# Optimization experiments

Measured on AMD Instinct MI355X. Metric: run time of the kernel, lower is better.

Reference implementation:

```python
import jax, jax.numpy as jnp
import numpy as np

LOG_STD_MAX = 2.0
LOG_STD_MIN = -5.0
N_EXPERTS = 16
TOPK = 4
OBS = 512
ACT = 256
BATCH = 16384


def setup_inputs() -> dict:
    key = jax.random.key(0)
    ks = jax.random.split(key, 7)
    s_obs = 1.0 / np.sqrt(OBS)
    return {
        "x": jax.random.normal(ks[0], (BATCH, OBS), dtype=jnp.float32),
        "router_w": jax.random.uniform(ks[1], (N_EXPERTS, OBS), jnp.float32, -s_obs, s_obs),
        "router_b": jax.random.uniform(ks[2], (N_EXPERTS,), jnp.float32, -s_obs, s_obs),
        "mean_w": jax.random.uniform(ks[3], (N_EXPERTS, ACT, OBS), jnp.float32, -s_obs, s_obs),
        "mean_b": jax.random.uniform(ks[4], (N_EXPERTS, ACT), jnp.float32, -s_obs, s_obs),
        "log_std_w": jax.random.uniform(ks[5], (N_EXPERTS, ACT, OBS), jnp.float32, -s_obs, s_obs),
        "log_std_b": jax.random.uniform(ks[6], (N_EXPERTS, ACT), jnp.float32, -s_obs, s_obs),
        "router_noise": 0,
    }


def reference(x, router_w, router_b, mean_w, mean_b, log_std_w, log_std_b, router_noise):
    # router_noise=0 -> deterministic path (training-time noise omitted)
    B = x.shape[0]
    router_logits = x @ router_w.T + router_b                    # [B, E]
    router_probs = jax.nn.softmax(router_logits, axis=-1)         # [B, E]
    topk_probs, topk_idx = jax.lax.top_k(router_probs, TOPK)      # [B, K]
    sparse_probs = jnp.zeros_like(router_probs).at[
        jnp.arange(B)[:, None], topk_idx
    ].set(topk_probs)                                             # [B, E]

    # all-expert dense stack: [B, E, A]
    expert_out = jnp.einsum("bo,eao->bea", x, mean_w) + mean_b
    log_std_out = jnp.einsum("bo,eao->bea", x, log_std_w) + log_std_b

    w = sparse_probs[:, :, None]                                  # [B, E, 1]
    mean = jnp.sum(expert_out * w, axis=1)                        # [B, A]
    log_std = jnp.sum(log_std_out * w, axis=1)                    # [B, A]
    log_std = jnp.tanh(log_std)
    log_std = LOG_STD_MIN + 0.5 * (LOG_STD_MAX - LOG_STD_MIN) * (log_std + 1.0)
    return mean, log_std
```

## Files before the change

kernel.cpp:

```cpp
#include <hip/hip_runtime.h>
#include <math.h>

#define BB   16384
#define OBS  512
#define NE   16
#define ACTD 256
#define TK   4

#define WS_ROWLIST_OFF  ((size_t)64)
#define WS_PROBLIST_OFF (WS_ROWLIST_OFF + (size_t)NE * BB * 4)
#define WS_SLOT_OFF     (WS_PROBLIST_OFF + (size_t)NE * BB * 4)
#define WS_XBF_OFF      (WS_SLOT_OFF + (size_t)NE * BB * 4)
#define WS_WM_OFF       (WS_XBF_OFF + (size_t)BB * OBS * 2)
#define WS_WL_OFF       (WS_WM_OFF + (size_t)NE * ACTD * OBS * 2)
#define WS_PART_OFF     (WS_WL_OFF + (size_t)NE * ACTD * OBS * 2)
#define WS_NEEDED_A2    (WS_PART_OFF + (size_t)2 * BB * TK * ACTD * 2)

typedef __attribute__((ext_vector_type(8))) short short8;
typedef __attribute__((ext_vector_type(4))) float floatx4;

__device__ __forceinline__ ushort f2bf(float f) {
    union { float f; unsigned u; } v; v.f = f;
    unsigned r = v.u + 0x7fffu + ((v.u >> 16) & 1u);
    return (ushort)(r >> 16);
}
__device__ __forceinline__ float bf2f(ushort u) {
    union { unsigned u; float f; } v; v.u = ((unsigned)u) << 16;
    return v.f;
}
__device__ __forceinline__ float lstd_act(float v) {
    return -5.f + 7.f * __builtin_amdgcn_rcpf(1.f + __expf(-2.f * v));
}

__global__ __launch_bounds__(256) void cvt2_bf16(
    const float* __restrict__ s0, const float* __restrict__ s1,
    ushort* __restrict__ d0, ushort* __restrict__ d1, int n4,
    int* __restrict__ counts)
{
    if (blockIdx.x == 0 && threadIdx.x < NE) counts[threadIdx.x] = 0;
    const int i = blockIdx.x * 256 + threadIdx.x;
    const float4* src = (i < n4) ? ((const float4*)s0 + i) : ((const float4*)s1 + (i - n4));
    ushort4* dst = (i < n4) ? ((ushort4*)d0 + i) : ((ushort4*)d1 + (i - n4));
    float4 v = *src;
    ushort4 o;
    o.x = f2bf(v.x); o.y = f2bf(v.y); o.z = f2bf(v.z); o.w = f2bf(v.w);
    *dst = o;
}

__global__ __launch_bounds__(256) void router_kernel(
    const float* __restrict__ x, const float* __restrict__ rw,
    const float* __restrict__ rb,
    int* __restrict__ counts, int* __restrict__ rowlist,
    float* __restrict__ problist, int* __restrict__ slot_of,
    ushort* __restrict__ xbf, int do_aux)
{
    __shared__ float wlds[NE * OBS];
    __shared__ int   lcnt[NE], lbase[NE];
    __shared__ int   s_e[64], s_lpos[64];
    __shared__ float s_p[64];

    const float4* rw4 = (const float4*)rw;
    float4* wl4 = (float4*)wlds;
    #pragma unroll
    for (int i = 0; i < 8; ++i) wl4[threadIdx.x + 256 * i] = rw4[threadIdx.x + 256 * i];
    if (threadIdx.x < NE) lcnt[threadIdx.x] = 0;
    __syncthreads();

    const int wave = threadIdx.x >> 6;
    const int lane = threadIdx.x & 63;
    const int q    = lane >> 4;
    const int i16  = lane & 15;
    const int row  = blockIdx.x * 16 + wave * 4 + q;

    const float4* xr = (const float4*)(x + (size_t)row * OBS);
    float4 xv[8];
    #pragma unroll
    for (int s = 0; s < 8; ++s) xv[s] = xr[s * 16 + i16];

    if (do_aux) {
        ushort4* xo = (ushort4*)(xbf + (size_t)row * OBS);
        #pragma unroll
        for (int s = 0; s < 8; ++s) {
            ushort4 o;
            o.x = f2bf(xv[s].x); o.y = f2bf(xv[s].y);
            o.z = f2bf(xv[s].z); o.w = f2bf(xv[s].w);
            xo[s * 16 + i16] = o;
        }
    }

    float p[NE];
    float m = -1e30f;
    #pragma unroll
    for (int e = 0; e < NE; ++e) {
        const float4* wep = (const float4*)(wlds + e * OBS);
        float d = 0.f;
        #pragma unroll
        for (int s = 0; s < 8; ++s) {
            float4 wv = wep[s * 16 + i16];
            d += xv[s].x * wv.x + xv[s].y * wv.y + xv[s].z * wv.z + xv[s].w * wv.w;
        }
        d += __shfl_xor(d, 1, 64);
        d += __shfl_xor(d, 2, 64);
        d += __shfl_xor(d, 4, 64);
        d += __shfl_xor(d, 8, 64);
        d += rb[e];
        p[e] = d;
        m = fmaxf(m, d);
    }
    float s = 0.f;
    #pragma unroll
    for (int e = 0; e < NE; ++e) { p[e] = __expf(p[e] - m); s += p[e]; }
    const float inv = 1.f / s;
    #pragma unroll
    for (int e = 0; e < NE; ++e) p[e] *= inv;

    int   sel_e[TK];
    float sel_p[TK];
    #pragma unroll
    for (int k = 0; k < TK; ++k) {
        float best = -1.f; int be = 0;
        #pragma unroll
        for (int e = 0; e < NE; ++e)
            if (p[e] > best) { best = p[e]; be = e; }
        sel_e[k] = be; sel_p[k] = best;
        #pragma unroll
        for (int e = 0; e < NE; ++e)
            if (e == be) p[e] = -2.f;
    }
    if (i16 < TK) {
        const int e = sel_e[i16];
        const int lpos = atomicAdd(&lcnt[e], 1);
        const int sid = (wave * 4 + q) * 4 + i16;
        s_e[sid] = e; s_p[sid] = sel_p[i16]; s_lpos[sid] = lpos;
    }
    __syncthreads();
    if (threadIdx.x < NE)
        lbase[threadIdx.x] = atomicAdd(&counts[threadIdx.x], lcnt[threadIdx.x]);
    __syncthreads();
    if (threadIdx.x < 64) {
        const int sid = threadIdx.x;
        const int e   = s_e[sid];
        const int pos = lbase[e] + s_lpos[sid];
        const int grow = blockIdx.x * 16 + (sid >> 2);
        rowlist[e * BB + pos]  = grow;
        problist[e * BB + pos] = s_p[sid];
        if (do_aux) slot_of[e * BB + pos] = grow * TK + (sid & 3);
    }
}

__global__ __launch_bounds__(256) void moe_gemm_64(
    const ushort* __restrict__ xbf,
    const ushort* __restrict__ wmean, const ushort* __restrict__ wlstd,
    const float* __restrict__ mean_b, const float* __restrict__ lstd_b,
    const int* __restrict__ counts, const int* __restrict__ rowlist,
    const float* __restrict__ problist, const int* __restrict__ slot_of,
    ushort* __restrict__ partial)
{
    const int flat = blockIdx.x + 256 * blockIdx.y + 4096 * blockIdx.z;
    const int virt = (flat & 7) * 2048 + (flat >> 3);
    const int zz    = virt & 3;
    const int tile0 = ((virt >> 2) & 255) * 64;
    const int e     = virt >> 10;

    const int cnt = counts[e];
    if (tile0 >= cnt) return;

    const int which = zz >> 1;
    const int ctile = (zz & 1) * 128;
    const ushort* W   = (which ? wlstd : wmean) + (size_t)e * ACTD * OBS;
    const float* bias = (which ? lstd_b : mean_b) + e * ACTD + ctile;
    ushort* Pp = partial + (size_t)which * BB * TK * ACTD;

    __shared__ __align__(16) ushort xls[64 * 64];
    __shared__ __align__(16) ushort wls[128 * 64];
    __shared__ int   idx_l[64];
    __shared__ float probs_l[64];

    const int tid = threadIdx.x;
    const int l   = tid & 63;
    const int w   = tid >> 6;

    if (tid < 64) {
        const int pos = tile0 + tid;
        const bool v = pos < cnt;
        probs_l[tid] = v ? problist[e * BB + pos] : 0.f;
        idx_l[tid]   = v ? slot_of[e * BB + pos] : -1;
    }

    const int c_sw = (l & 7) ^ (l >> 3);
    const ushort* xp[2];
    #pragma unroll
    for (int i = 0; i < 2; ++i) {
        const int lrow = 16 * w + 8 * i + (l >> 3);
        const int pos  = tile0 + lrow;
        const int grow = (pos < cnt) ? rowlist[e * BB + pos] : rowlist[e * BB + tile0];
        xp[i] = xbf + (size_t)grow * OBS + c_sw * 8;
    }
    const ushort* wp[4];
    #pragma unroll
    for (int j = 0; j < 4; ++j) {
        const int col = ctile + 32 * w + 8 * j + (l >> 3);
        wp[j] = W + (size_t)col * OBS + c_sw * 8;
    }

    const int wm  = (w >> 1) * 32;
    const int wn  = (w & 1) * 64;
    const int rlo = l & 15;
    const int q   = l >> 4;
    const int r7  = rlo & 7;

    floatx4 acc[2][4];
    #pragma unroll
    for (int mi = 0; mi < 2; ++mi)
        #pragma unroll
        for (int ni = 0; ni < 4; ++ni)
            acc[mi][ni] = (floatx4){0.f, 0.f, 0.f, 0.f};

    for (int kt = 0; kt < OBS; kt += 64) {
        __syncthreads();
        #pragma unroll
        for (int i = 0; i < 2; ++i)
            __builtin_amdgcn_global_load_lds(
                (const __attribute__((address_space(1))) unsigned int*)(xp[i] + kt),
                (__attribute__((address_space(3))) unsigned int*)(xls + (2 * w + i) * 512),
                16, 0, 0);
        #pragma unroll
        for (int j = 0; j < 4; ++j)
            __builtin_amdgcn_global_load_lds(
                (const __attribute__((address_space(1))) unsigned int*)(wp[j] + kt),
                (__attribute__((address_space(3))) unsigned int*)(wls + (4 * w + j) * 512),
                16, 0, 0);
        __syncthreads();

        #pragma unroll
        for (int ks = 0; ks < 2; ++ks) {
            const int ch = (4 * ks + q) ^ r7;
            short8 af[2], bfr[4];
            #pragma unroll
            for (int mi = 0; mi < 2; ++mi)
                af[mi] = *(const short8*)(xls + (wm + mi * 16 + rlo) * 64 + ch * 8);
            #pragma unroll
            for (int ni = 0; ni < 4; ++ni)
                bfr[ni] = *(const short8*)(wls + (wn + ni * 16 + rlo) * 64 + ch * 8);
            #pragma unroll
            for (int mi = 0; mi < 2; ++mi)
                #pragma unroll
                for (int ni = 0; ni < 4; ++ni)
                    acc[mi][ni] = __builtin_amdgcn_mfma_f32_16x16x32_bf16(
                        af[mi], bfr[ni], acc[mi][ni], 0, 0, 0);
        }
    }

    #pragma unroll
    for (int mi = 0; mi < 2; ++mi) {
        #pragma unroll
        for (int r = 0; r < 4; ++r) {
            const int lrow = wm + mi * 16 + q * 4 + r;
            const int slot = idx_l[lrow];
            if (slot < 0) continue;
            const float pw = probs_l[lrow];
            ushort* orow = Pp + (size_t)slot * ACTD + ctile + wn + rlo;
            #pragma unroll
            for (int ni = 0; ni < 4; ++ni)
                orow[ni * 16] = f2bf(pw * (acc[mi][ni][r] + bias[wn + ni * 16 + rlo]));
        }
    }
}

__global__ __launch_bounds__(256) void combine_kernel(
    const ushort* __restrict__ partial, float* __restrict__ out)
{
    const int t  = blockIdx.x * 256 + threadIdx.x;
    const int r  = t >> 6;
    const int c4 = (t & 63) * 4;
    const ushort* Pm = partial;
    const ushort* Pl = partial + (size_t)BB * TK * ACTD;

    float m0 = 0.f, m1 = 0.f, m2 = 0.f, m3 = 0.f;
    float l0 = 0.f, l1 = 0.f, l2 = 0.f, l3 = 0.f;
    #pragma unroll
    for (int k = 0; k < TK; ++k) {
        const size_t off = (size_t)(r * TK + k) * ACTD + c4;
        ushort4 vm = *(const ushort4*)(Pm + off);
        ushort4 vl = *(const ushort4*)(Pl + off);
        m0 += bf2f(vm.x); m1 += bf2f(vm.y); m2 += bf2f(vm.z); m3 += bf2f(vm.w);
        l0 += bf2f(vl.x); l1 += bf2f(vl.y); l2 += bf2f(vl.z); l3 += bf2f(vl.w);
    }
    float4 mo = make_float4(m0, m1, m2, m3);
    float4 lo = make_float4(lstd_act(l0), lstd_act(l1), lstd_act(l2), lstd_act(l3));
    *(float4*)(out + (size_t)r * ACTD + c4) = mo;
    *(float4*)(out + (size_t)BB * ACTD + (size_t)r * ACTD + c4) = lo;
}

__global__ __launch_bounds__(256) void moe_gemm_f32(
    const float* __restrict__ x,
    const float* __restrict__ mean_w, const float* __restrict__ mean_b,
    const float* __restrict__ lstd_w, const float* __restrict__ lstd_b,
    const int* __restrict__ counts, const int* __restrict__ rowlist,
    const float* __restrict__ problist, float* __restrict__ out)
{
    const int e = blockIdx.y;
    const int cnt = counts[e];
    const int tile0 = blockIdx.x * 32;
    if (tile0 >= cnt) return;

    const int zz    = blockIdx.z;
    const int which = zz >> 1;
    const int ctile = (zz & 1) * 128;
    const float* W    = (which ? lstd_w : mean_w) + (size_t)e * ACTD * OBS;
    const float* bias = (which ? lstd_b : mean_b) + e * ACTD;
    float* outp = out + (size_t)which * BB * ACTD;

    __shared__ float xls[32][32];
    __shared__ float wls[32][128];

    const int sr  = threadIdx.x >> 3;
    const int skq = threadIdx.x & 7;
    int stage_row = -1;
    {
        const int pos = tile0 + sr;
        if (pos < cnt) stage_row = rowlist[e * BB + pos];
    }

    const int r0 = (threadIdx.x >> 5) << 2;
    const int c0 = (threadIdx.x & 31) << 2;

    float acc[4][4] = {};

    for (int kt = 0; kt < OBS; kt += 32) {
        __syncthreads();
        {
            float4 v = make_float4(0.f, 0.f, 0.f, 0.f);
            if (stage_row >= 0)
                v = *(const float4*)(x + (size_t)stage_row * OBS + kt + skq * 4);
            xls[skq * 4 + 0][sr] = v.x;
            xls[skq * 4 + 1][sr] = v.y;
            xls[skq * 4 + 2][sr] = v.z;
            xls[skq * 4 + 3][sr] = v.w;
        }
        #pragma unroll
        for (int j = 0; j < 4; ++j) {
            const int i  = threadIdx.x + 256 * j;
            const int c  = i >> 3;
            const int kq = i & 7;
            float4 v = *(const float4*)(W + (size_t)(ctile + c) * OBS + kt + kq * 4);
            wls[kq * 4 + 0][c] = v.x;
            wls[kq * 4 + 1][c] = v.y;
            wls[kq * 4 + 2][c] = v.z;
            wls[kq * 4 + 3][c] = v.w;
        }
        __syncthreads();

        #pragma unroll
        for (int k = 0; k < 32; ++k) {
            const float4 xa = *(const float4*)&xls[k][r0];
            const float4 wb = *(const float4*)&wls[k][c0];
            const float xv[4] = { xa.x, xa.y, xa.z, xa.w };
            const float wv[4] = { wb.x, wb.y, wb.z, wb.w };
            #pragma unroll
            for (int i = 0; i < 4; ++i)
                #pragma unroll
                for (int j = 0; j < 4; ++j)
                    acc[i][j] = fmaf(xv[i], wv[j], acc[i][j]);
        }
    }

    #pragma unroll
    for (int i = 0; i < 4; ++i) {
        const int pos = tile0 + r0 + i;
        if (pos >= cnt) break;
        const int grow = rowlist[e * BB + pos];
        const float pw = problist[e * BB + pos];
        float* orow = outp + (size_t)grow * ACTD + ctile + c0;
        #pragma unroll
        for (int j = 0; j < 4; ++j)
            atomicAdd(&orow[j], pw * (acc[i][j] + bias[ctile + c0 + j]));
    }
}

__global__ __launch_bounds__(256) void tanh_ep(float* __restrict__ out)
{
    const int i = blockIdx.x * 256 + threadIdx.x;
    float4* p = (float4*)(out + (size_t)BB * ACTD);
    float4 v = p[i];
    v.x = -5.f + 3.5f * (tanhf(v.x) + 1.f);
    v.y = -5.f + 3.5f * (tanhf(v.y) + 1.f);
    v.z = -5.f + 3.5f * (tanhf(v.z) + 1.f);
    v.w = -5.f + 3.5f * (tanhf(v.w) + 1.f);
    p[i] = v;
}

extern "C" void kernel_launch(void* const* d_in, const int* in_sizes, int n_in,
                              void* d_out, int out_size, void* d_ws, size_t ws_size,
                              hipStream_t stream)
{
    const float* x        = (const float*)d_in[0];
    const float* router_w = (const float*)d_in[1];
    const float* router_b = (const float*)d_in[2];
    const float* mean_w   = (const float*)d_in[3];
    const float* mean_b   = (const float*)d_in[4];
    const float* lstd_w   = (const float*)d_in[5];
    const float* lstd_b   = (const float*)d_in[6];

    float* out = (float*)d_out;
    int*    counts   = (int*)d_ws;
    int*    rowlist  = (int*)((char*)d_ws + WS_ROWLIST_OFF);
    float*  problist = (float*)((char*)d_ws + WS_PROBLIST_OFF);
    int*    slot_of  = (int*)((char*)d_ws + WS_SLOT_OFF);
    ushort* xbf      = (ushort*)((char*)d_ws + WS_XBF_OFF);
    ushort* wmbf     = (ushort*)((char*)d_ws + WS_WM_OFF);
    ushort* wlbf     = (ushort*)((char*)d_ws + WS_WL_OFF);
    ushort* partial  = (ushort*)((char*)d_ws + WS_PART_OFF);

    const bool tierA2 = (ws_size >= WS_NEEDED_A2);

    if (tierA2) {
        const int wn4 = NE * ACTD * OBS / 4;
        cvt2_bf16<<<2 * wn4 / 256, 256, 0, stream>>>(mean_w, lstd_w, wmbf, wlbf,
                                                     wn4, counts);

        router_kernel<<<BB / 16, 256, 0, stream>>>(x, router_w, router_b,
                                                   counts, rowlist, problist,
                                                   slot_of, xbf, 1);

        dim3 grid(BB / 64, NE, 4);
        moe_gemm_64<<<grid, 256, 0, stream>>>(xbf, wmbf, wlbf, mean_b, lstd_b,
                                              counts, rowlist, problist,
                                              slot_of, partial);
        combine_kernel<<<BB * 64 / 256, 256, 0, stream>>>(partial, out);
    } else {
        hipMemsetAsync(d_ws, 0, 64, stream);
        hipMemsetAsync(d_out, 0, (size_t)out_size * sizeof(float), stream);
        router_kernel<<<BB / 16, 256, 0, stream>>>(x, router_w, router_b,
                                                   counts, rowlist, problist,
                                                   (int*)nullptr, (ushort*)nullptr, 0);
        dim3 grid(BB / 32, NE, 4);
        moe_gemm_f32<<<grid, 256, 0, stream>>>(x, mean_w, mean_b, lstd_w, lstd_b,
                                               counts, rowlist, problist, out);
        tanh_ep<<<(BB * ACTD / 4) / 256, 256, 0, stream>>>(out);
    }
}
```

Measured before the change: 207.3 us.

## Fuse weight bf16 conversion into router and compute mean/log_std in one GEMM block

Removes the separate weight-conversion kernel by folding the fp32-to-bf16 weight conversion into the router kernel and replacing the counts reset with a memset. The GEMM now computes both the mean and the log_std projections per block, sharing each loaded x tile across two weight tiles and two accumulator sets. This halves the number of GEMM blocks and the gathered x loads, at the cost of more registers and LDS per block, which may lower occupancy.

```diff
diff --git a/kernel.cpp b/kernel.cpp
--- a/kernel.cpp
+++ b/kernel.cpp
@@ -32,27 +32,14 @@
     return -5.f + 7.f * __builtin_amdgcn_rcpf(1.f + __expf(-2.f * v));
 }
 
-__global__ __launch_bounds__(256) void cvt2_bf16(
-    const float* __restrict__ s0, const float* __restrict__ s1,
-    ushort* __restrict__ d0, ushort* __restrict__ d1, int n4,
-    int* __restrict__ counts)
-{
-    if (blockIdx.x == 0 && threadIdx.x < NE) counts[threadIdx.x] = 0;
-    const int i = blockIdx.x * 256 + threadIdx.x;
-    const float4* src = (i < n4) ? ((const float4*)s0 + i) : ((const float4*)s1 + (i - n4));
-    ushort4* dst = (i < n4) ? ((ushort4*)d0 + i) : ((ushort4*)d1 + (i - n4));
-    float4 v = *src;
-    ushort4 o;
-    o.x = f2bf(v.x); o.y = f2bf(v.y); o.z = f2bf(v.z); o.w = f2bf(v.w);
-    *dst = o;
-}
-
 __global__ __launch_bounds__(256) void router_kernel(
     const float* __restrict__ x, const float* __restrict__ rw,
     const float* __restrict__ rb,
     int* __restrict__ counts, int* __restrict__ rowlist,
     float* __restrict__ problist, int* __restrict__ slot_of,
-    ushort* __restrict__ xbf, int do_aux)
+    ushort* __restrict__ xbf,
+    const float* __restrict__ mwf, const float* __restrict__ lwf,
+    ushort* __restrict__ wmbf, ushort* __restrict__ wlbf, int do_aux)
 {
     __shared__ float wlds[NE * OBS];
     __shared__ int   lcnt[NE], lbase[NE];
@@ -146,9 +133,29 @@
         problist[e * BB + pos] = s_p[sid];
         if (do_aux) slot_of[e * BB + pos] = grow * TK + (sid & 3);
     }
-}
-
-__global__ __launch_bounds__(256) void moe_gemm_64(
+
+    if (do_aux) {
+        const int gid = blockIdx.x * 256 + threadIdx.x;
+        const float4* m4 = (const float4*)mwf;
+        const float4* l4 = (const float4*)lwf;
+        ushort4* mo = (ushort4*)wmbf;
+        ushort4* lo = (ushort4*)wlbf;
+        #pragma unroll
+        for (int j = 0; j < 2; ++j) {
+            const int idx = gid + 262144 * j;
+            float4 a = m4[idx];
+            ushort4 oa;
+            oa.x = f2bf(a.x); oa.y = f2bf(a.y); oa.z = f2bf(a.z); oa.w = f2bf(a.w);
+            mo[idx] = oa;
+            float4 b = l4[idx];
+            ushort4 ob;
+            ob.x = f2bf(b.x); ob.y = f2bf(b.y); ob.z = f2bf(b.z); ob.w = f2bf(b.w);
+            lo[idx] = ob;
+        }
+    }
+}
+
+__global__ __launch_bounds__(256) void moe_gemm_2t(
     const ushort* __restrict__ xbf,
     const ushort* __restrict__ wmean, const ushort* __restrict__ wlstd,
     const float* __restrict__ mean_b, const float* __restrict__ lstd_b,
@@ -157,22 +164,25 @@
     ushort* __restrict__ partial)
 {
     const int flat = blockIdx.x + 256 * blockIdx.y + 4096 * blockIdx.z;
-    const int virt = (flat & 7) * 2048 + (flat >> 3);
-    const int zz    = virt & 3;
-    const int tile0 = ((virt >> 2) & 255) * 64;
-    const int e     = virt >> 10;
+    const int virt = (flat & 7) * 1024 + (flat >> 3);
+    const int zz    = virt & 1;
+    const int tile0 = ((virt >> 1) & 255) * 64;
+    const int e     = virt >> 9;
 
     const int cnt = counts[e];
     if (tile0 >= cnt) return;
 
-    const int which = zz >> 1;
-    const int ctile = (zz & 1) * 128;
-    const ushort* W   = (which ? wlstd : wmean) + (size_t)e * ACTD * OBS;
-    const float* bias = (which ? lstd_b : mean_b) + e * ACTD + ctile;
-    ushort* Pp = partial + (size_t)which * BB * TK * ACTD;
+    const int ctile = zz * 128;
+    const ushort* Wm = wmean + (size_t)e * ACTD * OBS;
+    const ushort* Wl = wlstd + (size_t)e * ACTD * OBS;
+    const float* bm  = mean_b + e * ACTD + ctile;
+    const float* bl  = lstd_b + e * ACTD + ctile;
+    ushort* PpM = partial;
+    ushort* PpL = partial + (size_t)BB * TK * ACTD;
 
     __shared__ __align__(16) ushort xls[64 * 64];
-    __shared__ __align__(16) ushort wls[128 * 64];
+    __shared__ __align__(16) ushort wmls[128 * 64];
+    __shared__ __align__(16) ushort wlls[128 * 64];
     __shared__ int   idx_l[64];
     __shared__ float probs_l[64];
 
@@ -196,25 +206,30 @@
         const int grow = (pos < cnt) ? rowlist[e * BB + pos] : rowlist[e * BB + tile0];
         xp[i] = xbf + (size_t)grow * OBS + c_sw * 8;
     }
-    const ushort* wp[4];
+    const ushort* wpm[4];
+    const ushort* wpl[4];
     #pragma unroll
     for (int j = 0; j < 4; ++j) {
         const int col = ctile + 32 * w + 8 * j + (l >> 3);
-        wp[j] = W + (size_t)col * OBS + c_sw * 8;
-    }
-
-    const int wm  = (w >> 1) * 32;
-    const int wn  = (w & 1) * 64;
-    const int rlo = l & 15;
-    const int q   = l >> 4;
-    const int r7  = rlo & 7;
-
-    floatx4 acc[2][4];
+        const size_t off = (size_t)col * OBS + c_sw * 8;
+        wpm[j] = Wm + off;
+        wpl[j] = Wl + off;
+    }
+
+    const int wm_  = (w >> 1) * 32;
+    const int wn   = (w & 1) * 64;
+    const int rlo  = l & 15;
+    const int q    = l >> 4;
+    const int r7   = rlo & 7;
+
+    floatx4 accM[2][4], accL[2][4];
     #pragma unroll
     for (int mi = 0; mi < 2; ++mi)
         #pragma unroll
-        for (int ni = 0; ni < 4; ++ni)
-            acc[mi][ni] = (floatx4){0.f, 0.f, 0.f, 0.f};
+        for (int ni = 0; ni < 4; ++ni) {
+            accM[mi][ni] = (floatx4){0.f, 0.f, 0.f, 0.f};
+            accL[mi][ni] = (floatx4){0.f, 0.f, 0.f, 0.f};
+        }
 
     for (int kt = 0; kt < OBS; kt += 64) {
         __syncthreads();
@@ -227,8 +242,14 @@
         #pragma unroll
         for (int j = 0; j < 4; ++j)
             __builtin_amdgcn_global_load_lds(
-                (const __attribute__((address_space(1))) unsigned int*)(wp[j] + kt),
-                (__attribute__((address_space(3))) unsigned int*)(wls + (4 * w + j) * 512),
+                (const __attribute__((address_space(1))) unsigned int*)(wpm[j] + kt),
+                (__attribute__((address_space(3))) unsigned int*)(wmls + (4 * w + j) * 512),
+                16, 0, 0);
+        #pragma unroll
+        for (int j = 0; j < 4; ++j)
+            __builtin_amdgcn_global_load_lds(
+                (const __attribute__((address_space(1))) unsigned int*)(wpl[j] + kt),
+                (__attribute__((address_space(3))) unsigned int*)(wlls + (4 * w + j) * 512),
                 16, 0, 0);
         __syncthreads();
 
@@ -238,16 +259,25 @@
             short8 af[2], bfr[4];
             #pragma unroll
             for (int mi = 0; mi < 2; ++mi)
-                af[mi] = *(const short8*)(xls + (wm + mi * 16 + rlo) * 64 + ch * 8);
+                af[mi] = *(const short8*)(xls + (wm_ + mi * 16 + rlo) * 64 + ch * 8);
             #pragma unroll
             for (int ni = 0; ni < 4; ++ni)
-                bfr[ni] = *(const short8*)(wls + (wn + ni * 16 + rlo) * 64 + ch * 8);
+                bfr[ni] = *(const short8*)(wmls + (wn + ni * 16 + rlo) * 64 + ch * 8);
             #pragma unroll
             for (int mi = 0; mi < 2; ++mi)
                 #pragma unroll
                 for (int ni = 0; ni < 4; ++ni)
-                    acc[mi][ni] = __builtin_amdgcn_mfma_f32_16x16x32_bf16(
-                        af[mi], bfr[ni], acc[mi][ni], 0, 0, 0);
+                    accM[mi][ni] = __builtin_amdgcn_mfma_f32_16x16x32_bf16(
+                        af[mi], bfr[ni], accM[mi][ni], 0, 0, 0);
+            #pragma unroll
+            for (int ni = 0; ni < 4; ++ni)
+                bfr[ni] = *(const short8*)(wlls + (wn + ni * 16 + rlo) * 64 + ch * 8);
+            #pragma unroll
+            for (int mi = 0; mi < 2; ++mi)
+                #pragma unroll
+                for (int ni = 0; ni < 4; ++ni)
+                    accL[mi][ni] = __builtin_amdgcn_mfma_f32_16x16x32_bf16(
+                        af[mi], bfr[ni], accL[mi][ni], 0, 0, 0);
         }
     }
 
@@ -255,14 +285,18 @@
     for (int mi = 0; mi < 2; ++mi) {
         #pragma unroll
         for (int r = 0; r < 4; ++r) {
-            const int lrow = wm + mi * 16 + q * 4 + r;
+            const int lrow = wm_ + mi * 16 + q * 4 + r;
             const int slot = idx_l[lrow];
             if (slot < 0) continue;
             const float pw = probs_l[lrow];
-            ushort* orow = Pp + (size_t)slot * ACTD + ctile + wn + rlo;
-            #pragma unroll
-            for (int ni = 0; ni < 4; ++ni)
-                orow[ni * 16] = f2bf(pw * (acc[mi][ni][r] + bias[wn + ni * 16 + rlo]));
+            const size_t obase = (size_t)slot * ACTD + ctile + wn + rlo;
+            ushort* orm = PpM + obase;
+            ushort* orl = PpL + obase;
+            #pragma unroll
+            for (int ni = 0; ni < 4; ++ni) {
+                orm[ni * 16] = f2bf(pw * (accM[mi][ni][r] + bm[wn + ni * 16 + rlo]));
+                orl[ni * 16] = f2bf(pw * (accL[mi][ni][r] + bl[wn + ni * 16 + rlo]));
+            }
         }
     }
 }
@@ -415,16 +449,15 @@
     const bool tierA2 = (ws_size >= WS_NEEDED_A2);
 
     if (tierA2) {
-        const int wn4 = NE * ACTD * OBS / 4;
-        cvt2_bf16<<<2 * wn4 / 256, 256, 0, stream>>>(mean_w, lstd_w, wmbf, wlbf,
-                                                     wn4, counts);
+        hipMemsetAsync(d_ws, 0, 64, stream);
 
         router_kernel<<<BB / 16, 256, 0, stream>>>(x, router_w, router_b,
                                                    counts, rowlist, problist,
-                                                   slot_of, xbf, 1);
-
-        dim3 grid(BB / 64, NE, 4);
-        moe_gemm_64<<<grid, 256, 0, stream>>>(xbf, wmbf, wlbf, mean_b, lstd_b,
+                                                   slot_of, xbf,
+                                                   mean_w, lstd_w, wmbf, wlbf, 1);
+
+        dim3 grid(BB / 64, NE, 2);
+        moe_gemm_2t<<<grid, 256, 0, stream>>>(xbf, wmbf, wlbf, mean_b, lstd_b,
                                               counts, rowlist, problist,
                                               slot_of, partial);
         combine_kernel<<<BB * 64 / 256, 256, 0, stream>>>(partial, out);
@@ -433,7 +466,10 @@
         hipMemsetAsync(d_out, 0, (size_t)out_size * sizeof(float), stream);
         router_kernel<<<BB / 16, 256, 0, stream>>>(x, router_w, router_b,
                                                    counts, rowlist, problist,
-                                                   (int*)nullptr, (ushort*)nullptr, 0);
+                                                   (int*)nullptr, (ushort*)nullptr,
+                                                   (const float*)nullptr,
+                                                   (const float*)nullptr,
+                                                   (ushort*)nullptr, (ushort*)nullptr, 0);
         dim3 grid(BB / 32, NE, 4);
         moe_gemm_f32<<<grid, 256, 0, stream>>>(x, mean_w, mean_b, lstd_w, lstd_b,
                                                counts, rowlist, problist, out);
```

After: 214.6 us. +3.5%, slower.
